# Kernel optimization log

Hardware: AMD Instinct MI355X
Metric: run time of the kernel (lower is better)

Reference implementation:

```python
import jax, jax.numpy as jnp
import numpy as np

B, N, HL, D, HID, O, E, S, K = 8, 64, 32, 256, 1024, 256, 8, 3, 2


def setup_inputs() -> dict:
    key = jax.random.key(0)
    ks = jax.random.split(key, 12)
    w = 0.02
    return {
        "feature_vectors": jax.random.normal(ks[0], (B, N, HL, D), dtype=jnp.float32),
        "object_types": jax.random.uniform(ks[1], (B, N, HL, S, 1), dtype=jnp.float32),
        "gate_w": jax.random.normal(ks[2], (D, E), dtype=jnp.float32) * w,
        "gate_b": jnp.zeros((E,), dtype=jnp.float32),
        "shared_w1": jax.random.normal(ks[3], (S, D, HID), dtype=jnp.float32) * w,
        "shared_b1": jnp.zeros((S, HID), dtype=jnp.float32),
        "shared_w2": jax.random.normal(ks[4], (S, HID, O), dtype=jnp.float32) * w,
        "shared_b2": jnp.zeros((S, O), dtype=jnp.float32),
        "ind_w1": jax.random.normal(ks[5], (E, D, HID), dtype=jnp.float32) * w,
        "ind_b1": jnp.zeros((E, HID), dtype=jnp.float32),
        "ind_w2": jax.random.normal(ks[6], (E, HID, O), dtype=jnp.float32) * w,
        "ind_b2": jnp.zeros((E, O), dtype=jnp.float32),
    }


def reference(feature_vectors, object_types, gate_w, gate_b,
              shared_w1, shared_b1, shared_w2, shared_b2,
              ind_w1, ind_b1, ind_w2, ind_b2):
    b, n, hl, d = feature_vectors.shape
    x = feature_vectors.reshape(-1, d)                      # (T, D)
    T = x.shape[0]

    # gating: softmax -> top-k -> renormalize selected probs
    gates = jax.nn.softmax(x @ gate_w + gate_b, axis=-1)    # (T, E)
    vals, idx = jax.lax.top_k(gates, K)                     # (T, K)
    w = vals / vals.sum(axis=-1, keepdims=True)
    # dense (T, E) combine weights: zero outside top-k, equivalent to scatter-add loop
    w_full = jnp.zeros_like(gates).at[jnp.arange(T)[:, None], idx].set(w)

    # shared experts: all S experts on every token, weighted by object_types
    sh_h = jax.nn.relu(jnp.einsum('td,sdh->tsh', x, shared_w1) + shared_b1)
    sh_o = jnp.einsum('tsh,sho->tso', sh_h, shared_w2) + shared_b2  # (T, S, O)
    obj = object_types.reshape(-1, S, 1)                    # (T, S, 1)
    shared_out = (sh_o * obj).sum(axis=1)                   # (T, O)

    # independent experts: dense all-expert GEMM, combined by masked gate weights
    ih = jax.nn.relu(jnp.einsum('td,edh->teh', x, ind_w1) + ind_b1)
    io = jnp.einsum('teh,eho->teo', ih, ind_w2) + ind_b2    # (T, E, O)
    ind_out = jnp.einsum('te,teo->to', w_full, io)          # (T, O)

    out = 0.5 * shared_out + 0.5 * ind_out
    return out.reshape(b, n, hl, -1)
```

## Files before the change

### kernel.cpp

```cpp
#include <hip/hip_runtime.h>
#include <hip/hip_bf16.h>
#include <stdint.h>

#define TOK   16384
#define DIM   256
#define HIDN  1024
#define OUTD  256
#define NEXP  8
#define NSH   3
#define NSLOT 11
#define TM    64
#define NCH   32
#define HSTR  40

typedef short bf16x8  __attribute__((ext_vector_type(8)));
typedef float f32x4   __attribute__((ext_vector_type(4)));
typedef short short4v __attribute__((ext_vector_type(4)));

constexpr size_t XB_OFF   = 0;
constexpr size_t W1P_OFF  = XB_OFF  + (size_t)TOK*DIM*2;
constexpr size_t W2P_OFF  = W1P_OFF + (size_t)NSLOT*DIM*HIDN*2;
constexpr size_t WTS_OFF  = W2P_OFF + (size_t)NSLOT*HIDN*OUTD*2;
constexpr size_t IDS_OFF  = WTS_OFF + (size_t)TOK*2*4;
constexpr size_t CNT_OFF  = IDS_OFF + (size_t)TOK*2*4;
constexpr size_t LTOK_OFF = CNT_OFF + 256;
constexpr size_t LW_OFF   = LTOK_OFF + (size_t)NEXP*TOK*4;
constexpr size_t WS_NEED  = LW_OFF + (size_t)NEXP*TOK*4;

__device__ __forceinline__ unsigned short f2bf(float f) {
    __hip_bfloat16 h = __float2bfloat16(f);
    return *reinterpret_cast<unsigned short*>(&h);
}

__device__ __forceinline__ f32x4 mfma16(bf16x8 a, bf16x8 b, f32x4 c) {
    return __builtin_amdgcn_mfma_f32_16x16x32_bf16(a, b, c, 0, 0, 0);
}

__device__ __forceinline__ void gload_lds16(const void* g, void* l) {
    __builtin_amdgcn_global_load_lds(
        (const __attribute__((address_space(1))) unsigned int*)g,
        (__attribute__((address_space(3))) unsigned int*)l, 16, 0, 0);
}

__device__ __forceinline__ void fence_sched() { __builtin_amdgcn_sched_barrier(0); }

__global__ __launch_bounds__(256) void k_prep(
    const float* __restrict__ x, const float* __restrict__ gw,
    const float* __restrict__ gb, short* __restrict__ xb,
    float* __restrict__ wts, int* __restrict__ ids) {
    int wid = threadIdx.x >> 6, lane = threadIdx.x & 63;
    int t = blockIdx.x * 4 + wid;
    const float* xr = x + (size_t)t * DIM;
    {
        float4 v = reinterpret_cast<const float4*>(xr)[lane];
        short4v o;
        o[0] = (short)f2bf(v.x); o[1] = (short)f2bf(v.y);
        o[2] = (short)f2bf(v.z); o[3] = (short)f2bf(v.w);
        reinterpret_cast<short4v*>(xb + (size_t)t * DIM)[lane] = o;
    }
    float acc[NEXP] = {0.f,0.f,0.f,0.f,0.f,0.f,0.f,0.f};
    #pragma unroll
    for (int i = 0; i < DIM/64; ++i) {
        int d = i*64 + lane;
        float xv = xr[d];
        const float* g = gw + (size_t)d * NEXP;
        #pragma unroll
        for (int e = 0; e < NEXP; ++e) acc[e] = fmaf(xv, g[e], acc[e]);
    }
    #pragma unroll
    for (int off = 32; off; off >>= 1) {
        #pragma unroll
        for (int e = 0; e < NEXP; ++e) acc[e] += __shfl_xor(acc[e], off, 64);
    }
    if (lane == 0) {
        float l[NEXP];
        #pragma unroll
        for (int e = 0; e < NEXP; ++e) l[e] = acc[e] + gb[e];
        int e0 = 0; float v0 = l[0];
        #pragma unroll
        for (int e = 1; e < NEXP; ++e) if (l[e] > v0) { v0 = l[e]; e0 = e; }
        int e1 = -1; float v1 = -1e30f;
        #pragma unroll
        for (int e = 0; e < NEXP; ++e) if (e != e0 && l[e] > v1) { v1 = l[e]; e1 = e; }
        float r = expf(v1 - v0);
        float w0 = 0.5f / (1.f + r);
        float w1 = 0.5f * r / (1.f + r);
        ids[2*t]   = e0;  ids[2*t+1] = e1;
        wts[2*t]   = w0;  wts[2*t+1] = w1;
    }
}

__global__ __launch_bounds__(256) void k_convert_w(
    const float* __restrict__ sw1, const float* __restrict__ iw1,
    const float* __restrict__ sw2, const float* __restrict__ iw2,
    short* __restrict__ w1p, short* __restrict__ w2p) {
    __shared__ float tile[32][68];
    int bid = blockIdx.x, tid = threadIdx.x;
    const int W1B = NSLOT * 8 * 16;
    bool isW1 = bid < W1B;
    int b = isW1 ? bid : bid - W1B;
    int NTG = isW1 ? 16 : 4;
    int KT  = isW1 ? 8 : 32;
    int NT  = isW1 ? 64 : 16;
    int Nd  = isW1 ? HIDN : OUTD;
    int ntg = b % NTG; b /= NTG;
    int kt  = b % KT;
    int slot = b / KT;
    const float* src;
    if (isW1) src = (slot < NSH) ? sw1 + (size_t)slot*DIM*HIDN  : iw1 + (size_t)(slot-NSH)*DIM*HIDN;
    else      src = (slot < NSH) ? sw2 + (size_t)slot*HIDN*OUTD : iw2 + (size_t)(slot-NSH)*HIDN*OUTD;
    {
        int tr = tid >> 3, tc = (tid & 7) * 8;
        const float* s = src + (size_t)(kt*32 + tr)*Nd + ntg*64 + tc;
        float4 v0 = *reinterpret_cast<const float4*>(s);
        float4 v1 = *reinterpret_cast<const float4*>(s + 4);
        *reinterpret_cast<float4*>(&tile[tr][tc])     = v0;
        *reinterpret_cast<float4*>(&tile[tr][tc + 4]) = v1;
    }
    __syncthreads();
    {
        int ntl = tid >> 6, lane = tid & 63;
        int n  = ntl*16 + (lane & 15);
        int k8 = (lane >> 4) * 8;
        bf16x8 o;
        #pragma unroll
        for (int j = 0; j < 8; ++j) o[j] = (short)f2bf(tile[k8 + j][n]);
        size_t gidx = (((size_t)slot*KT + kt)*NT + ntg*4 + ntl)*64 + lane;
        short* dst = isW1 ? w1p : w2p;
        reinterpret_cast<bf16x8*>(dst)[gidx] = o;
    }
}

__global__ __launch_bounds__(256) void k_route(
    const int* __restrict__ ids, const float* __restrict__ wts,
    int* __restrict__ cnt, int* __restrict__ ltok, float* __restrict__ lw) {
    __shared__ int lcnt[NEXP];
    __shared__ int gbase[NEXP];
    int tid = threadIdx.x;
    if (tid < NEXP) lcnt[tid] = 0;
    __syncthreads();
    int t = blockIdx.x * 256 + tid;
    int e0 = ids[2*t], e1 = ids[2*t+1];
    int p0 = atomicAdd(&lcnt[e0], 1);
    int p1 = atomicAdd(&lcnt[e1], 1);
    __syncthreads();
    if (tid < NEXP) gbase[tid] = atomicAdd(&cnt[tid], lcnt[tid]);
    __syncthreads();
    size_t o0 = (size_t)e0*TOK + gbase[e0] + p0;
    size_t o1 = (size_t)e1*TOK + gbase[e1] + p1;
    ltok[o0] = t;  lw[o0] = wts[2*t];
    ltok[o1] = t;  lw[o1] = wts[2*t+1];
}

__global__ __launch_bounds__(512) void k_moe(
    const short* __restrict__ xb, const short* __restrict__ w1p, const short* __restrict__ w2p,
    const float* __restrict__ sb1, const float* __restrict__ sb2,
    const float* __restrict__ ib1, const float* __restrict__ ib2,
    const float* __restrict__ obj, const int* __restrict__ cnt,
    const int* __restrict__ ltok, const float* __restrict__ lw,
    float* __restrict__ out)
{
    __shared__ __align__(16) char Wb1[16384];
    __shared__ __align__(16) char Wb2[16384];
    __shared__ __align__(16) short Hs[TM * HSTR];
    __shared__ float bias_lds[HIDN];
    __shared__ int   tokl[TM];
    __shared__ float twl[TM];

    const int slot = blockIdx.y;
    const int m0   = blockIdx.x * TM;
    const bool sh  = slot < NSH;
    const int e    = slot - NSH;
    int count = TOK;
    if (!sh) { count = cnt[e]; if (m0 >= count) return; }

    const int tid  = threadIdx.x;
    const int w    = tid >> 6, lane = tid & 63;
    const int wm   = w >> 1,   wn   = w & 1;
    const int pm   = w >> 2,   pn   = w & 3;
    const int lrow = lane & 15, g   = lane >> 4;

    if (tid < TM) {
        if (sh) {
            tokl[tid] = m0 + tid;
            twl[tid]  = 0.5f * obj[(size_t)(m0 + tid)*NSH + slot];
        } else {
            int p = m0 + tid;
            bool ok = p < count;
            tokl[tid] = ok ? ltok[(size_t)e*TOK + p] : 0;
            twl[tid]  = ok ? lw[(size_t)e*TOK + p] : 0.f;
        }
    }
    __syncthreads();

    const char* w1base = (const char*)w1p;
    const char* w2base = (const char*)w2p;
    const float* b1v = sh ? (sb1 + slot*HIDN) : (ib1 + (size_t)e*HIDN);

    const int tokA = tokl[wm*16 + lrow];
    bf16x8 areg[8];
    #pragma unroll
    for (int kt = 0; kt < 8; ++kt)
        areg[kt] = *reinterpret_cast<const bf16x8*>(
            xb + (size_t)tokA*DIM + kt*32 + g*8);

    if (w < 4)
        gload_lds16((const char*)b1v + w*1024 + lane*16, (char*)bias_lds + w*1024);

    auto stage_w1 = [&](int c) {
        #pragma unroll
        for (int i = 0; i < 2; ++i)
            gload_lds16(
                w1base + ((((size_t)slot*8 + w)*64 + c*2 + i) << 10) + lane*16,
                Wb1 + ((w*2 + i) << 10));
    };
    auto stage_w2 = [&](int c) {
        const char* s2 = w2base + ((((size_t)slot*32 + c)*16) << 10);
        #pragma unroll
        for (int i = 0; i < 2; ++i)
            gload_lds16(s2 + ((w*2 + i) << 10) + lane*16, Wb2 + ((w*2 + i) << 10));
    };
    stage_w1(0);
    stage_w2(0);
    asm volatile("s_waitcnt vmcnt(0) lgkmcnt(0)" ::: "memory");
    __syncthreads();

    f32x4 acc2[2][4] = {};
    for (int c = 0; c < NCH; ++c) {
        if (c > 0) {
            stage_w2(c);
            fence_sched();
            asm volatile("s_waitcnt vmcnt(2)" ::: "memory");
            fence_sched();
            __builtin_amdgcn_s_barrier();
            fence_sched();
        }

        f32x4 acc1 = {};
        #pragma unroll
        for (int kt = 0; kt < 8; ++kt) {
            bf16x8 b = *reinterpret_cast<const bf16x8*>(
                Wb1 + ((kt*2 + wn) << 10) + lane*16);
            acc1 = mfma16(areg[kt], b, acc1);
        }
        {
            int col = wn*16 + lrow;
            float bias = bias_lds[c*32 + col];
            #pragma unroll
            for (int r = 0; r < 4; ++r) {
                int row = wm*16 + g*4 + r;
                float v = fmaxf(acc1[r] + bias, 0.f) * twl[row];
                Hs[row*HSTR + col] = (short)f2bf(v);
            }
        }
        fence_sched();
        asm volatile("s_waitcnt lgkmcnt(0)" ::: "memory");
        fence_sched();
        __builtin_amdgcn_s_barrier();
        fence_sched();

        if (c + 1 < NCH) stage_w1(c + 1);
        fence_sched();
        if (c + 1 < NCH) { asm volatile("s_waitcnt vmcnt(2)" ::: "memory"); }
        else             { asm volatile("s_waitcnt vmcnt(0)" ::: "memory"); }
        fence_sched();
        __builtin_amdgcn_s_barrier();
        fence_sched();

        {
            bf16x8 a2[2];
            #pragma unroll
            for (int mf = 0; mf < 2; ++mf)
                a2[mf] = *reinterpret_cast<const bf16x8*>(
                    Hs + (pm*32 + mf*16 + lrow)*HSTR + g*8);
            #pragma unroll
            for (int nf = 0; nf < 4; ++nf) {
                bf16x8 b2 = *reinterpret_cast<const bf16x8*>(
                    Wb2 + ((pn*4 + nf) << 10) + lane*16);
                #pragma unroll
                for (int mf = 0; mf < 2; ++mf)
                    acc2[mf][nf] = mfma16(a2[mf], b2, acc2[mf][nf]);
            }
        }
        fence_sched();
        __builtin_amdgcn_s_barrier();
        fence_sched();
    }

    {
        const float* b2 = sh ? (sb2 + slot*OUTD) : (ib2 + (size_t)e*OUTD);
        #pragma unroll
        for (int mf = 0; mf < 2; ++mf)
            #pragma unroll
            for (int nf = 0; nf < 4; ++nf) {
                int col = pn*64 + nf*16 + lrow;
                #pragma unroll
                for (int r = 0; r < 4; ++r) {
                    int row = pm*32 + mf*16 + g*4 + r;
                    if (sh || (m0 + row < count)) {
                        int t = tokl[row];
                        float v = acc2[mf][nf][r] + twl[row] * b2[col];
                        atomicAdd(&out[(size_t)t*OUTD + col], v);
                    }
                }
            }
    }
}

extern "C" void kernel_launch(void* const* d_in, const int* in_sizes, int n_in,
                              void* d_out, int out_size, void* d_ws, size_t ws_size,
                              hipStream_t stream) {
    const float* x   = (const float*)d_in[0];
    const float* obj = (const float*)d_in[1];
    const float* gw  = (const float*)d_in[2];
    const float* gb  = (const float*)d_in[3];
    const float* sw1 = (const float*)d_in[4];
    const float* sb1 = (const float*)d_in[5];
    const float* sw2 = (const float*)d_in[6];
    const float* sb2 = (const float*)d_in[7];
    const float* iw1 = (const float*)d_in[8];
    const float* ib1 = (const float*)d_in[9];
    const float* iw2 = (const float*)d_in[10];
    const float* ib2 = (const float*)d_in[11];
    float* out = (float*)d_out;
    char* ws = (char*)d_ws;
    if (ws_size < WS_NEED) return;

    short* xb   = (short*)(ws + XB_OFF);
    short* w1p  = (short*)(ws + W1P_OFF);
    short* w2p  = (short*)(ws + W2P_OFF);
    float* wts  = (float*)(ws + WTS_OFF);
    int*   ids  = (int*)  (ws + IDS_OFF);
    int*   cnt  = (int*)  (ws + CNT_OFF);
    int*   ltok = (int*)  (ws + LTOK_OFF);
    float* lwt  = (float*)(ws + LW_OFF);

    hipMemsetAsync(ws + CNT_OFF, 0, 256, stream);
    hipMemsetAsync(out, 0, (size_t)out_size * 4, stream);
    k_prep<<<TOK/4, 256, 0, stream>>>(x, gw, gb, xb, wts, ids);
    k_convert_w<<<NSLOT*8*16 + NSLOT*32*4, 256, 0, stream>>>(sw1, iw1, sw2, iw2, w1p, w2p);
    k_route<<<TOK/256, 256, 0, stream>>>(ids, wts, cnt, ltok, lwt);
    k_moe<<<dim3(TOK/TM, NSLOT), 512, 0, stream>>>(
        xb, w1p, w2p, sb1, sb2, ib1, ib2, obj, cnt, ltok, lwt, out);
}
```

Baseline: 206.0 us.

## Double-buffer W1/W2 LDS tiles and prefetch two chunks ahead

Gives each expert weight tile (W1 and W2) two LDS buffers. The next W2 chunk and the W1 chunk two ahead now stream in while the current chunk is being computed, which drops one barrier and one wait per loop iteration. The intent is to hide global-load latency behind the MFMA work. The cost is twice the weight-staging LDS, about 74KB per block, which may lower the number of resident blocks per CU.

```diff
diff --git a/kernel.cpp b/kernel.cpp
--- a/kernel.cpp
+++ b/kernel.cpp
@@ -160,8 +160,8 @@
     const int* __restrict__ ltok, const float* __restrict__ lw,
     float* __restrict__ out)
 {
-    __shared__ __align__(16) char Wb1[16384];
-    __shared__ __align__(16) char Wb2[16384];
+    __shared__ __align__(16) char Wb1[2][16384];
+    __shared__ __align__(16) char Wb2[2][16384];
     __shared__ __align__(16) short Hs[TM * HSTR];
     __shared__ float bias_lds[HIDN];
     __shared__ int   tokl[TM];
@@ -207,40 +207,47 @@
     if (w < 4)
         gload_lds16((const char*)b1v + w*1024 + lane*16, (char*)bias_lds + w*1024);
 
-    auto stage_w1 = [&](int c) {
+    auto stage_w1 = [&](int c, int buf) {
         #pragma unroll
         for (int i = 0; i < 2; ++i)
             gload_lds16(
                 w1base + ((((size_t)slot*8 + w)*64 + c*2 + i) << 10) + lane*16,
-                Wb1 + ((w*2 + i) << 10));
+                Wb1[buf] + ((w*2 + i) << 10));
     };
-    auto stage_w2 = [&](int c) {
+    auto stage_w2 = [&](int c, int buf) {
         const char* s2 = w2base + ((((size_t)slot*32 + c)*16) << 10);
         #pragma unroll
         for (int i = 0; i < 2; ++i)
-            gload_lds16(s2 + ((w*2 + i) << 10) + lane*16, Wb2 + ((w*2 + i) << 10));
+            gload_lds16(s2 + ((w*2 + i) << 10) + lane*16, Wb2[buf] + ((w*2 + i) << 10));
     };
-    stage_w1(0);
-    stage_w2(0);
+
     asm volatile("s_waitcnt vmcnt(0) lgkmcnt(0)" ::: "memory");
     __syncthreads();
+
+    stage_w1(0, 0);
+    stage_w2(0, 0);
+    stage_w1(1, 1);
 
     f32x4 acc2[2][4] = {};
     for (int c = 0; c < NCH; ++c) {
-        if (c > 0) {
-            stage_w2(c);
+        const int p = c & 1;
+        if (c + 1 < NCH) {
+            stage_w2(c + 1, p ^ 1);
             fence_sched();
-            asm volatile("s_waitcnt vmcnt(2)" ::: "memory");
+            asm volatile("s_waitcnt vmcnt(4)" ::: "memory");
+        } else {
             fence_sched();
-            __builtin_amdgcn_s_barrier();
-            fence_sched();
-        }
+            asm volatile("s_waitcnt vmcnt(0)" ::: "memory");
+        }
+        fence_sched();
+        __builtin_amdgcn_s_barrier();
+        fence_sched();
 
         f32x4 acc1 = {};
         #pragma unroll
         for (int kt = 0; kt < 8; ++kt) {
             bf16x8 b = *reinterpret_cast<const bf16x8*>(
-                Wb1 + ((kt*2 + wn) << 10) + lane*16);
+                Wb1[p] + ((kt*2 + wn) << 10) + lane*16);
             acc1 = mfma16(areg[kt], b, acc1);
         }
         {
@@ -259,12 +266,7 @@
         __builtin_amdgcn_s_barrier();
         fence_sched();
 
-        if (c + 1 < NCH) stage_w1(c + 1);
-        fence_sched();
-        if (c + 1 < NCH) { asm volatile("s_waitcnt vmcnt(2)" ::: "memory"); }
-        else             { asm volatile("s_waitcnt vmcnt(0)" ::: "memory"); }
-        fence_sched();
-        __builtin_amdgcn_s_barrier();
+        if (c + 2 < NCH) stage_w1(c + 2, p);
         fence_sched();
 
         {
@@ -276,7 +278,7 @@
             #pragma unroll
             for (int nf = 0; nf < 4; ++nf) {
                 bf16x8 b2 = *reinterpret_cast<const bf16x8*>(
-                    Wb2 + ((pn*4 + nf) << 10) + lane*16);
+                    Wb2[p] + ((pn*4 + nf) << 10) + lane*16);
                 #pragma unroll
                 for (int mf = 0; mf < 2; ++mf)
                     acc2[mf][nf] = mfma16(a2[mf], b2, acc2[mf][nf]);
```

After: 203.8 us. Within noise of the previous version (-1.1%).

## Halve MoE block to 4 waves with larger per-wave tiles and 64-wide hidden chunks

Applied to the files above, without the earlier changes.

The fused MoE kernel now runs 256 threads per block instead of 512. Each wave computes a 32x32 tile of the first GEMM and a 32x128 tile of the second GEMM. The hidden dimension is processed in 16 chunks of 64 rather than 32 chunks of 32, with LDS weight buffers doubled and the H tile stride widened. This cuts the number of barriers and raises MFMA work per LDS fragment load. In exchange, register pressure per wave rises, LDS per block grows to about 75KB, and fewer waves per CU are available to hide latency.

```diff
diff --git a/kernel.cpp b/kernel.cpp
--- a/kernel.cpp
+++ b/kernel.cpp
@@ -10,8 +10,8 @@
 #define NSH   3
 #define NSLOT 11
 #define TM    64
-#define NCH   32
-#define HSTR  40
+#define NCH   16
+#define HSTR  72
 
 typedef short bf16x8  __attribute__((ext_vector_type(8)));
 typedef float f32x4   __attribute__((ext_vector_type(4)));
@@ -152,7 +152,7 @@
     ltok[o1] = t;  lw[o1] = wts[2*t+1];
 }
 
-__global__ __launch_bounds__(512) void k_moe(
+__global__ __launch_bounds__(256) void k_moe(
     const short* __restrict__ xb, const short* __restrict__ w1p, const short* __restrict__ w2p,
     const float* __restrict__ sb1, const float* __restrict__ sb2,
     const float* __restrict__ ib1, const float* __restrict__ ib2,
@@ -160,8 +160,8 @@
     const int* __restrict__ ltok, const float* __restrict__ lw,
     float* __restrict__ out)
 {
-    __shared__ __align__(16) char Wb1[16384];
-    __shared__ __align__(16) char Wb2[16384];
+    __shared__ __align__(16) char Wb1[32768];
+    __shared__ __align__(16) char Wb2[32768];
     __shared__ __align__(16) short Hs[TM * HSTR];
     __shared__ float bias_lds[HIDN];
     __shared__ int   tokl[TM];
@@ -177,7 +177,6 @@
     const int tid  = threadIdx.x;
     const int w    = tid >> 6, lane = tid & 63;
     const int wm   = w >> 1,   wn   = w & 1;
-    const int pm   = w >> 2,   pn   = w & 3;
     const int lrow = lane & 15, g   = lane >> 4;
 
     if (tid < TM) {
@@ -197,86 +196,108 @@
     const char* w2base = (const char*)w2p;
     const float* b1v = sh ? (sb1 + slot*HIDN) : (ib1 + (size_t)e*HIDN);
 
-    const int tokA = tokl[wm*16 + lrow];
-    bf16x8 areg[8];
+    const int tokA0 = tokl[wm*32 + 0*16 + lrow];
+    const int tokA1 = tokl[wm*32 + 1*16 + lrow];
+    bf16x8 areg[2][8];
     #pragma unroll
-    for (int kt = 0; kt < 8; ++kt)
-        areg[kt] = *reinterpret_cast<const bf16x8*>(
-            xb + (size_t)tokA*DIM + kt*32 + g*8);
-
-    if (w < 4)
-        gload_lds16((const char*)b1v + w*1024 + lane*16, (char*)bias_lds + w*1024);
+    for (int kt = 0; kt < 8; ++kt) {
+        areg[0][kt] = *reinterpret_cast<const bf16x8*>(
+            xb + (size_t)tokA0*DIM + kt*32 + g*8);
+        areg[1][kt] = *reinterpret_cast<const bf16x8*>(
+            xb + (size_t)tokA1*DIM + kt*32 + g*8);
+    }
+
+    gload_lds16((const char*)b1v + w*1024 + lane*16, (char*)bias_lds + w*1024);
 
     auto stage_w1 = [&](int c) {
         #pragma unroll
-        for (int i = 0; i < 2; ++i)
+        for (int i = 0; i < 8; ++i) {
+            int idx = w*8 + i;
             gload_lds16(
-                w1base + ((((size_t)slot*8 + w)*64 + c*2 + i) << 10) + lane*16,
-                Wb1 + ((w*2 + i) << 10));
+                w1base + ((((size_t)slot*8 + (idx >> 2))*64 + c*4 + (idx & 3)) << 10) + lane*16,
+                Wb1 + (idx << 10));
+        }
     };
     auto stage_w2 = [&](int c) {
-        const char* s2 = w2base + ((((size_t)slot*32 + c)*16) << 10);
-        #pragma unroll
-        for (int i = 0; i < 2; ++i)
-            gload_lds16(s2 + ((w*2 + i) << 10) + lane*16, Wb2 + ((w*2 + i) << 10));
+        const char* s2 = w2base + ((((size_t)slot*32 + c*2)*16) << 10);
+        #pragma unroll
+        for (int i = 0; i < 8; ++i) {
+            int idx = w*8 + i;
+            gload_lds16(s2 + (idx << 10) + lane*16, Wb2 + (idx << 10));
+        }
     };
+
     stage_w1(0);
     stage_w2(0);
     asm volatile("s_waitcnt vmcnt(0) lgkmcnt(0)" ::: "memory");
     __syncthreads();
 
-    f32x4 acc2[2][4] = {};
+    f32x4 acc2[2][8] = {};
     for (int c = 0; c < NCH; ++c) {
         if (c > 0) {
             stage_w2(c);
             fence_sched();
-            asm volatile("s_waitcnt vmcnt(2)" ::: "memory");
+            asm volatile("s_waitcnt vmcnt(8)" ::: "memory");
             fence_sched();
             __builtin_amdgcn_s_barrier();
             fence_sched();
         }
 
-        f32x4 acc1 = {};
+        f32x4 acc1[2][2] = {};
         #pragma unroll
         for (int kt = 0; kt < 8; ++kt) {
-            bf16x8 b = *reinterpret_cast<const bf16x8*>(
-                Wb1 + ((kt*2 + wn) << 10) + lane*16);
-            acc1 = mfma16(areg[kt], b, acc1);
-        }
-        {
-            int col = wn*16 + lrow;
-            float bias = bias_lds[c*32 + col];
-            #pragma unroll
-            for (int r = 0; r < 4; ++r) {
-                int row = wm*16 + g*4 + r;
-                float v = fmaxf(acc1[r] + bias, 0.f) * twl[row];
-                Hs[row*HSTR + col] = (short)f2bf(v);
+            bf16x8 b0 = *reinterpret_cast<const bf16x8*>(
+                Wb1 + ((kt*4 + wn*2 + 0) << 10) + lane*16);
+            bf16x8 b1 = *reinterpret_cast<const bf16x8*>(
+                Wb1 + ((kt*4 + wn*2 + 1) << 10) + lane*16);
+            #pragma unroll
+            for (int mf = 0; mf < 2; ++mf) {
+                acc1[mf][0] = mfma16(areg[mf][kt], b0, acc1[mf][0]);
+                acc1[mf][1] = mfma16(areg[mf][kt], b1, acc1[mf][1]);
             }
         }
+        #pragma unroll
+        for (int nf = 0; nf < 2; ++nf) {
+            int col = (wn*2 + nf)*16 + lrow;
+            float bias = bias_lds[c*64 + col];
+            #pragma unroll
+            for (int mf = 0; mf < 2; ++mf)
+                #pragma unroll
+                for (int r = 0; r < 4; ++r) {
+                    int row = wm*32 + mf*16 + g*4 + r;
+                    float v = fmaxf(acc1[mf][nf][r] + bias, 0.f) * twl[row];
+                    Hs[row*HSTR + col] = (short)f2bf(v);
+                }
+        }
         fence_sched();
         asm volatile("s_waitcnt lgkmcnt(0)" ::: "memory");
         fence_sched();
         __builtin_amdgcn_s_barrier();
         fence_sched();
 
-        if (c + 1 < NCH) stage_w1(c + 1);
-        fence_sched();
-        if (c + 1 < NCH) { asm volatile("s_waitcnt vmcnt(2)" ::: "memory"); }
-        else             { asm volatile("s_waitcnt vmcnt(0)" ::: "memory"); }
+        if (c + 1 < NCH) {
+            stage_w1(c + 1);
+            fence_sched();
+            asm volatile("s_waitcnt vmcnt(8)" ::: "memory");
+        } else {
+            fence_sched();
+            asm volatile("s_waitcnt vmcnt(0)" ::: "memory");
+        }
         fence_sched();
         __builtin_amdgcn_s_barrier();
         fence_sched();
 
-        {
+        #pragma unroll
+        for (int k2 = 0; k2 < 2; ++k2) {
             bf16x8 a2[2];
             #pragma unroll
             for (int mf = 0; mf < 2; ++mf)
                 a2[mf] = *reinterpret_cast<const bf16x8*>(
-                    Hs + (pm*32 + mf*16 + lrow)*HSTR + g*8);
-            #pragma unroll
-            for (int nf = 0; nf < 4; ++nf) {
+                    Hs + (wm*32 + mf*16 + lrow)*HSTR + k2*32 + g*8);
+            #pragma unroll
+            for (int nf = 0; nf < 8; ++nf) {
                 bf16x8 b2 = *reinterpret_cast<const bf16x8*>(
-                    Wb2 + ((pn*4 + nf) << 10) + lane*16);
+                    Wb2 + ((k2*16 + wn*8 + nf) << 10) + lane*16);
                 #pragma unroll
                 for (int mf = 0; mf < 2; ++mf)
                     acc2[mf][nf] = mfma16(a2[mf], b2, acc2[mf][nf]);
@@ -292,11 +313,11 @@
         #pragma unroll
         for (int mf = 0; mf < 2; ++mf)
             #pragma unroll
-            for (int nf = 0; nf < 4; ++nf) {
-                int col = pn*64 + nf*16 + lrow;
+            for (int nf = 0; nf < 8; ++nf) {
+                int col = wn*128 + nf*16 + lrow;
                 #pragma unroll
                 for (int r = 0; r < 4; ++r) {
-                    int row = pm*32 + mf*16 + g*4 + r;
+                    int row = wm*32 + mf*16 + g*4 + r;
                     if (sh || (m0 + row < count)) {
                         int t = tokl[row];
                         float v = acc2[mf][nf][r] + twl[row] * b2[col];
@@ -340,6 +361,6 @@
     k_prep<<<TOK/4, 256, 0, stream>>>(x, gw, gb, xb, wts, ids);
     k_convert_w<<<NSLOT*8*16 + NSLOT*32*4, 256, 0, stream>>>(sw1, iw1, sw2, iw2, w1p, w2p);
     k_route<<<TOK/256, 256, 0, stream>>>(ids, wts, cnt, ltok, lwt);
-    k_moe<<<dim3(TOK/TM, NSLOT), 512, 0, stream>>>(
+    k_moe<<<dim3(TOK/TM, NSLOT), 256, 0, stream>>>(
         xb, w1p, w2p, sb1, sb2, ib1, ib2, obj, cnt, ltok, lwt, out);
 }
```

New measurement: 229.6 us. 1.11x slower.
